# Optimization experiments

Measured on AMD Instinct MI355X. Metric: run time of the kernel, lower is better.

Reference implementation:

```python
import jax, jax.numpy as jnp
import numpy as np

B, P = 8, 1024
NUM_BINS = 11


def setup_inputs() -> dict:
    key = jax.random.key(0)
    x = jax.random.normal(key, (B, P, 6), dtype=jnp.float32)
    return {"x": x, "num_bins": NUM_BINS}


def reference(x, num_bins):
    Bv, Pv, _ = x.shape
    eps = 1e-6
    pos = x[..., 0:3]            # [B,P,3]
    ori = x[..., 3:6]            # [B,P,3]

    # axis 1 = i (source point), axis 2 = j (pair point)
    delta = pos[:, None, :, :] - pos[:, :, None, :]          # pj - pi: [B,P,P,3]
    ni = ori[:, :, None, :]                                   # [B,P,1,3]
    nj = ori[:, None, :, :]                                   # [B,1,P,3]

    dist = jnp.sqrt(jnp.sum(delta * delta, axis=-1))          # [B,P,P]

    ni_b = jnp.broadcast_to(ni, delta.shape)
    v = jnp.cross(delta, ni_b, axis=-1)
    v = v / (jnp.linalg.norm(v, axis=-1, keepdims=True) + eps)
    w = jnp.cross(ni_b, v, axis=-1)
    w = w / (jnp.linalg.norm(w, axis=-1, keepdims=True) + eps)

    alpha = jnp.sum(v * nj, axis=-1)                          # [B,P,P]
    phi = jnp.sum(ni * delta, axis=-1) / (dist + eps)         # [B,P,P]
    theta = jnp.arctan2(jnp.sum(w * nj, axis=-1),
                        jnp.sum(ni * nj, axis=-1)) / jnp.pi   # [B,P,P]

    def to_idx(a):
        # map [-1,1] -> bin index, truncation toward zero like torch .to(int64)
        idx = ((a + 1.0) * 0.5 * num_bins).astype(jnp.int32)
        return jnp.minimum(idx, num_bins - 1)

    fpfh_idx = (to_idx(alpha) * num_bins + to_idx(phi)) * num_bins + to_idx(theta)
    fpfh_idx = fpfh_idx.reshape(Bv, Pv * Pv)                  # [B, P*P]

    # exclude diagonal (i == j) pairs via zero weight, equivalent to the
    # eye-masked gather in the original (diagonal entries are finite)
    offdiag = (1.0 - jnp.eye(Pv, dtype=jnp.float32)).reshape(Pv * Pv)
    weights = jnp.broadcast_to(offdiag, (Bv, Pv * Pv))

    num_dim_feat = num_bins * num_bins * num_bins
    freq = jnp.zeros((Bv, num_dim_feat), dtype=jnp.float32)
    freq = freq.at[jnp.arange(Bv)[:, None], fpfh_idx].add(weights)
    freq = freq / (Pv * (Pv - 1))
    return freq
```

## Files before the change

### kernel.cpp

```cpp
#include <hip/hip_runtime.h>

#define P 1024
#define NB 11
#define NBINS 1331
#define BATCH 8
#define TI 8

#define RFL(f) __uint_as_float(__builtin_amdgcn_readfirstlane(__float_as_uint(f)))

__global__ __launch_bounds__(256) void fpfh_zero(int* __restrict__ hist) {
    int i = blockIdx.x * 256 + threadIdx.x;
    if (i < BATCH * NBINS) hist[i] = 0;
}

__global__ __launch_bounds__(256) void fpfh_main(const float* __restrict__ x,
                                                 int* __restrict__ ghist) {
    __shared__ int shist[NBINS];

    const int t  = threadIdx.x;
    const int b  = blockIdx.y;
    const int i0 = blockIdx.x * TI;
    const float* xb = x + b * (P * 6);

    for (int k = t; k < NBINS; k += 256) shist[k] = 0;

    float PIX[TI], PIY[TI], PIZ[TI], NIX[TI], NIY[TI], NIZ[TI], NII[TI], SNI[TI];
    #pragma unroll
    for (int il = 0; il < TI; ++il) {
        const float* xi = xb + (i0 + il) * 6;
        PIX[il] = RFL(xi[0]); PIY[il] = RFL(xi[1]); PIZ[il] = RFL(xi[2]);
        NIX[il] = RFL(xi[3]); NIY[il] = RFL(xi[4]); NIZ[il] = RFL(xi[5]);
        float nii = fmaf(NIX[il], NIX[il],
                    fmaf(NIY[il], NIY[il], NIZ[il] * NIZ[il]));
        NII[il] = RFL(nii);
        SNI[il] = RFL(__builtin_amdgcn_sqrtf(nii));
    }

    float pjx[4], pjy[4], pjz[4], njx[4], njy[4], njz[4];
    #pragma unroll
    for (int jt = 0; jt < 4; ++jt) {
        const float* xj = xb + (jt * 256 + t) * 6;
        pjx[jt] = xj[0]; pjy[jt] = xj[1]; pjz[jt] = xj[2];
        njx[jt] = xj[3]; njy[jt] = xj[4]; njz[jt] = xj[5];
    }

    __syncthreads();

    const float C1 = 0.959492973614497f,  S1 = 0.281732556841430f;
    const float C2 = 0.654860733945285f,  S2 = 0.755749574354258f;
    const float C3 = 0.142314838273285f,  S3 = 0.989821441880933f;
    const float C4 = -0.415415013001886f, S4 = 0.909631995354518f;
    const float C5 = -0.841253532831181f, S5 = 0.540640817455598f;

    #pragma unroll
    for (int jt = 0; jt < 4; ++jt) {
        const int j = jt * 256 + t;

        #pragma unroll
        for (int il = 0; il < TI; ++il) {
            const float dx = pjx[jt] - PIX[il];
            const float dy = pjy[jt] - PIY[il];
            const float dz = pjz[jt] - PIZ[il];

            const float dd    = fmaf(dx, dx, fmaf(dy, dy, dz * dz));
            const float nid   = fmaf(NIX[il], dx, fmaf(NIY[il], dy, NIZ[il] * dz));
            const float nidnj = fmaf(NIX[il], njx[jt],
                                fmaf(NIY[il], njy[jt], NIZ[il] * njz[jt]));
            const float ddnj  = fmaf(dx, njx[jt], fmaf(dy, njy[jt], dz * njz[jt]));

            const float cvx = fmaf(dy, NIZ[il], -dz * NIY[il]);
            const float cvy = fmaf(dz, NIX[il], -dx * NIZ[il]);
            const float cvz = fmaf(dx, NIY[il], -dy * NIX[il]);
            const float cvdnj = fmaf(cvx, njx[jt],
                                fmaf(cvy, njy[jt], cvz * njz[jt]));

            float cvv = fmaf(dd, NII[il], -nid * nid);
            cvv = fmaxf(cvv, 0.0f);
            const float rsq_cvv = __builtin_amdgcn_rsqf(cvv);
            const float alpha = cvdnj * rsq_cvv;
            const float scv   = cvv * rsq_cvv;

            const float phi = nid * __builtin_amdgcn_rsqf(dd);

            const float y_t = fmaf(NII[il], ddnj, -nid * nidnj);
            const float x_t = (SNI[il] * nidnj) * scv;
            const float ay  = __builtin_fabsf(y_t);

            int k = (fmaf(ay, C1, -x_t * S1) > 0.0f)
                  + (fmaf(ay, C2, -x_t * S2) > 0.0f)
                  + (fmaf(ay, C3, -x_t * S3) > 0.0f)
                  + (fmaf(ay, C4, -x_t * S4) > 0.0f)
                  + (fmaf(ay, C5, -x_t * S5) > 0.0f);
            const int ith = (y_t < 0.0f) ? 5 - k : 5 + k;

            int ia = (int)fmaf(alpha, 5.5f, 5.5f); ia = min(ia, NB - 1);
            int ip = (int)fmaf(phi,   5.5f, 5.5f); ip = min(ip, NB - 1);

            int bin = (ia * NB + ip) * NB + ith;
            if (bin < 0) bin += NBINS;
            if ((j != i0 + il) && ((unsigned)bin < (unsigned)NBINS))
                atomicAdd(&shist[bin], 1);
        }
    }
    __syncthreads();

    int* gb = ghist + b * NBINS;
    for (int k = t; k < NBINS; k += 256) {
        int c = shist[k];
        if (c) atomicAdd(&gb[k], c);
    }
}

__global__ __launch_bounds__(256) void fpfh_convert(const int* __restrict__ hist,
                                                    float* __restrict__ out) {
    int i = blockIdx.x * 256 + threadIdx.x;
    if (i < BATCH * NBINS)
        out[i] = (float)hist[i] / 1047552.0f;
}

extern "C" void kernel_launch(void* const* d_in, const int* in_sizes, int n_in,
                              void* d_out, int out_size, void* d_ws, size_t ws_size,
                              hipStream_t stream) {
    const float* x = (const float*)d_in[0];
    float* out = (float*)d_out;
    int* hist = (int*)d_ws;

    const int nOut = BATCH * NBINS;
    fpfh_zero<<<(nOut + 255) / 256, 256, 0, stream>>>(hist);
    dim3 grid(P / TI, BATCH);
    fpfh_main<<<grid, 256, 0, stream>>>(x, hist);
    fpfh_convert<<<(nOut + 255) / 256, 256, 0, stream>>>(hist, out);
}
```

Baseline: 30.97 us.

## Write per-block partial histograms and reduce them, replacing global atomics and zero kernel

Each block now writes its shared-memory histogram to its own slot in the workspace instead of doing global atomics. A reduction kernel sums all partial slots and normalises, so the zeroing kernel is dropped when the workspace is large enough. The theta binning also changes from five fma comparisons to one reciprocal followed by tangent-threshold comparisons. The trade-off is a reduce kernel that reads 128 slots per batch, and the approximate reciprocal may move values near bin edges into a different bin.

```diff
diff --git a/kernel.cpp b/kernel.cpp
--- a/kernel.cpp
+++ b/kernel.cpp
@@ -5,16 +5,13 @@
 #define NBINS 1331
 #define BATCH 8
 #define TI 8
+#define NBLK (P / TI)
 
 #define RFL(f) __uint_as_float(__builtin_amdgcn_readfirstlane(__float_as_uint(f)))
 
-__global__ __launch_bounds__(256) void fpfh_zero(int* __restrict__ hist) {
-    int i = blockIdx.x * 256 + threadIdx.x;
-    if (i < BATCH * NBINS) hist[i] = 0;
-}
-
 __global__ __launch_bounds__(256) void fpfh_main(const float* __restrict__ x,
-                                                 int* __restrict__ ghist) {
+                                                 int* __restrict__ part,
+                                                 int npart) {
     __shared__ int shist[NBINS];
 
     const int t  = threadIdx.x;
@@ -22,7 +19,7 @@
     const int i0 = blockIdx.x * TI;
     const float* xb = x + b * (P * 6);
 
-    for (int k = t; k < NBINS; k += 256) shist[k] = 0;
+    for (int z = t; z < NBINS; z += 256) shist[z] = 0;
 
     float PIX[TI], PIY[TI], PIZ[TI], NIX[TI], NIY[TI], NIZ[TI], NII[TI], SNI[TI];
     #pragma unroll
@@ -30,8 +27,7 @@
         const float* xi = xb + (i0 + il) * 6;
         PIX[il] = RFL(xi[0]); PIY[il] = RFL(xi[1]); PIZ[il] = RFL(xi[2]);
         NIX[il] = RFL(xi[3]); NIY[il] = RFL(xi[4]); NIZ[il] = RFL(xi[5]);
-        float nii = fmaf(NIX[il], NIX[il],
-                    fmaf(NIY[il], NIY[il], NIZ[il] * NIZ[il]));
+        float nii = fmaf(NIX[il], NIX[il], fmaf(NIY[il], NIY[il], NIZ[il] * NIZ[il]));
         NII[il] = RFL(nii);
         SNI[il] = RFL(__builtin_amdgcn_sqrtf(nii));
     }
@@ -45,12 +41,6 @@
     }
 
     __syncthreads();
-
-    const float C1 = 0.959492973614497f,  S1 = 0.281732556841430f;
-    const float C2 = 0.654860733945285f,  S2 = 0.755749574354258f;
-    const float C3 = 0.142314838273285f,  S3 = 0.989821441880933f;
-    const float C4 = -0.415415013001886f, S4 = 0.909631995354518f;
-    const float C5 = -0.841253532831181f, S5 = 0.540640817455598f;
 
     #pragma unroll
     for (int jt = 0; jt < 4; ++jt) {
@@ -68,33 +58,28 @@
                                 fmaf(NIY[il], njy[jt], NIZ[il] * njz[jt]));
             const float ddnj  = fmaf(dx, njx[jt], fmaf(dy, njy[jt], dz * njz[jt]));
 
-            const float cvx = fmaf(dy, NIZ[il], -dz * NIY[il]);
-            const float cvy = fmaf(dz, NIX[il], -dx * NIZ[il]);
-            const float cvz = fmaf(dx, NIY[il], -dy * NIX[il]);
+            const float cvx = fmaf(dy, NIZ[il], -(dz * NIY[il]));
+            const float cvy = fmaf(dz, NIX[il], -(dx * NIZ[il]));
+            const float cvz = fmaf(dx, NIY[il], -(dy * NIX[il]));
             const float cvdnj = fmaf(cvx, njx[jt],
                                 fmaf(cvy, njy[jt], cvz * njz[jt]));
 
-            float cvv = fmaf(dd, NII[il], -nid * nid);
-            cvv = fmaxf(cvv, 0.0f);
-            const float rsq_cvv = __builtin_amdgcn_rsqf(cvv);
-            const float alpha = cvdnj * rsq_cvv;
-            const float scv   = cvv * rsq_cvv;
+            float cvv = fmaxf(fmaf(dd, NII[il], -(nid * nid)), 0.0f);
+            const float rs    = __builtin_amdgcn_rsqf(cvv);
+            const float alpha = cvdnj * rs;
+            const float scv   = cvv * rs;
 
             const float phi = nid * __builtin_amdgcn_rsqf(dd);
 
-            const float y_t = fmaf(NII[il], ddnj, -nid * nidnj);
+            const float y_t = fmaf(NII[il], ddnj, -(nid * nidnj));
             const float x_t = (SNI[il] * nidnj) * scv;
-            const float ay  = __builtin_fabsf(y_t);
+            const float tq  = x_t * __builtin_amdgcn_rcpf(__builtin_fabsf(y_t));
+            int kk = (tq <  3.40568625f) + (tq <  0.86650494f) + (tq < 0.14377830f)
+                   + (tq < -0.45668469f) + (tq < -1.55603037f);
+            const int ith = (y_t < 0.0f) ? 5 - kk : 5 + kk;
 
-            int k = (fmaf(ay, C1, -x_t * S1) > 0.0f)
-                  + (fmaf(ay, C2, -x_t * S2) > 0.0f)
-                  + (fmaf(ay, C3, -x_t * S3) > 0.0f)
-                  + (fmaf(ay, C4, -x_t * S4) > 0.0f)
-                  + (fmaf(ay, C5, -x_t * S5) > 0.0f);
-            const int ith = (y_t < 0.0f) ? 5 - k : 5 + k;
-
-            int ia = (int)fmaf(alpha, 5.5f, 5.5f); ia = min(ia, NB - 1);
-            int ip = (int)fmaf(phi,   5.5f, 5.5f); ip = min(ip, NB - 1);
+            int ia = min((int)fmaf(alpha, 5.5f, 5.5f), NB - 1);
+            int ip = min((int)fmaf(phi,   5.5f, 5.5f), NB - 1);
 
             int bin = (ia * NB + ip) * NB + ith;
             if (bin < 0) bin += NBINS;
@@ -104,18 +89,30 @@
     }
     __syncthreads();
 
-    int* gb = ghist + b * NBINS;
-    for (int k = t; k < NBINS; k += 256) {
-        int c = shist[k];
-        if (c) atomicAdd(&gb[k], c);
+    if (npart == NBLK) {
+        int* slot = part + (b * NBLK + blockIdx.x) * NBINS;
+        for (int z = t; z < NBINS; z += 256) slot[z] = shist[z];
+    } else {
+        int* slot = part + (b * npart + (blockIdx.x % npart)) * NBINS;
+        for (int z = t; z < NBINS; z += 256) {
+            int c = shist[z];
+            if (c) atomicAdd(&slot[z], c);
+        }
     }
 }
 
-__global__ __launch_bounds__(256) void fpfh_convert(const int* __restrict__ hist,
-                                                    float* __restrict__ out) {
-    int i = blockIdx.x * 256 + threadIdx.x;
-    if (i < BATCH * NBINS)
-        out[i] = (float)hist[i] / 1047552.0f;
+__global__ __launch_bounds__(256) void fpfh_reduce(const int* __restrict__ part,
+                                                   float* __restrict__ out,
+                                                   int npart) {
+    const int idx = blockIdx.x * 256 + threadIdx.x;
+    if (idx >= BATCH * NBINS) return;
+    const int b   = idx / NBINS;
+    const int bin = idx - b * NBINS;
+    const int* p  = part + b * npart * NBINS + bin;
+    int s = 0;
+    #pragma unroll 8
+    for (int k = 0; k < npart; ++k) s += p[k * NBINS];
+    out[idx] = (float)s * (1.0f / 1047552.0f);
 }
 
 extern "C" void kernel_launch(void* const* d_in, const int* in_sizes, int n_in,
@@ -123,11 +120,23 @@
                               hipStream_t stream) {
     const float* x = (const float*)d_in[0];
     float* out = (float*)d_out;
-    int* hist = (int*)d_ws;
+    int* part  = (int*)d_ws;
+
+    const size_t slot_bytes = (size_t)BATCH * NBINS * sizeof(int);
+    const size_t full_need  = slot_bytes * NBLK;
+    int npart;
+    if (ws_size >= full_need) {
+        npart = NBLK;
+    } else {
+        npart = (int)(ws_size / slot_bytes);
+        if (npart < 1)   npart = 1;
+        if (npart > NBLK) npart = NBLK;
+        hipMemsetAsync(d_ws, 0, slot_bytes * npart, stream);
+    }
+
+    dim3 grid(NBLK, BATCH);
+    fpfh_main<<<grid, 256, 0, stream>>>(x, part, npart);
 
     const int nOut = BATCH * NBINS;
-    fpfh_zero<<<(nOut + 255) / 256, 256, 0, stream>>>(hist);
-    dim3 grid(P / TI, BATCH);
-    fpfh_main<<<grid, 256, 0, stream>>>(x, hist);
-    fpfh_convert<<<(nOut + 255) / 256, 256, 0, stream>>>(hist, out);
+    fpfh_reduce<<<(nOut + 255) / 256, 256, 0, stream>>>(part, out, npart);
 }
```

New measurement: 28.91 us. 6.7% less time.
